# Optimization experiments

Hardware: AMD Instinct MI355X
Metric: run time of the kernel (lower is better)

The kernel has to match this reference:

```python
import jax, jax.numpy as jnp
import numpy as np

B = 32768   # batch
D = 1024    # input_dimension
H = 2048    # hidden width (layer_sizes = [2048, 2048])
LN_EPS = 1e-5


def _layer_norm(h, g, b):
    m = jnp.mean(h, axis=-1, keepdims=True)
    v = jnp.var(h, axis=-1, keepdims=True)
    return (h - m) * jax.lax.rsqrt(v + LN_EPS) * g + b


def setup_inputs() -> dict:
    key = jax.random.key(0)
    ks = jax.random.split(key, 5)
    s1 = 1.0 / np.sqrt(D)
    s2 = 1.0 / np.sqrt(H)
    return {
        "x": jax.random.normal(ks[0], (B, D), dtype=jnp.float32),
        "W1": jax.random.uniform(ks[1], (D, H), jnp.float32, -s1, s1),
        "b1": jax.random.uniform(ks[2], (H,), jnp.float32, -s1, s1),
        "g1": jnp.ones((H,), jnp.float32),
        "be1": jnp.zeros((H,), jnp.float32),
        "W2": jax.random.uniform(ks[3], (H, 9), jnp.float32, -s2, s2),
        "b2": jax.random.uniform(ks[4], (9,), jnp.float32, -s2, s2),
        "g2": jnp.ones((9,), jnp.float32),
        "be2": jnp.zeros((9,), jnp.float32),
    }


def reference(x, W1, b1, g1, be1, W2, b2, g2, be2):
    # MLP: Linear -> ReLU -> LayerNorm, twice (final width 9)
    h = _layer_norm(jax.nn.relu(x @ W1 + b1), g1, be1)      # [B, H]
    r = _layer_norm(jax.nn.relu(h @ W2 + b2), g2, be2)      # [B, 9]
    R = r.reshape(x.shape[0], 3, 3)                          # [B, 3, 3]
    # SVD projection onto SO(3): U @ diag(1,1,det(U Vh)) @ Vh
    U, _, Vh = jnp.linalg.svd(R, full_matrices=False)
    d = jnp.linalg.det(U @ Vh)                               # [B]
    scale = jnp.stack([jnp.ones_like(d), jnp.ones_like(d), d], axis=-1)  # [B,3]
    return (U * scale[:, None, :]) @ Vh                      # scale last col of U
```

## Files before the change

### kernel.cpp

```cpp
#include <hip/hip_runtime.h>

typedef unsigned short u16;
typedef _Float16 f16x8 __attribute__((ext_vector_type(8)));
typedef float f32x4 __attribute__((ext_vector_type(4)));

#define GLD16(gptr, lptr)                                                              \
  __builtin_amdgcn_global_load_lds((const __attribute__((address_space(1))) void*)(gptr), \
                                   (__attribute__((address_space(3))) void*)(lptr), 16, 0, 0)

#define MFMA_F16(a, b, c) __builtin_amdgcn_mfma_f32_16x16x32_f16((a), (b), (c), 0, 0, 0)

__global__ __launch_bounds__(256) void k_split_w1t(const float* __restrict__ w1,
                                                   u16* __restrict__ wh, u16* __restrict__ wl) {
  __shared__ float tile[32][33];
  int bn = blockIdx.x & 63;
  int bk = blockIdx.x >> 6;
  int tn = threadIdx.x & 31, tq = threadIdx.x >> 5;
#pragma unroll
  for (int r = 0; r < 4; ++r) {
    int k = bk * 32 + tq + r * 8;
    tile[tq + r * 8][tn] = w1[(size_t)k * 2048 + bn * 32 + tn];
  }
  __syncthreads();
#pragma unroll
  for (int r = 0; r < 4; ++r) {
    int n = bn * 32 + tq + r * 8;
    float v = tile[tn][tq + r * 8];
    _Float16 hi = (_Float16)v;
    _Float16 lo = (_Float16)(v - (float)hi);
    int qp = (tn >> 3) ^ ((n >> 1) & 3);
    int kp = bk * 32 + qp * 8 + (tn & 7);
    wh[(size_t)n * 1024 + kp] = __builtin_bit_cast(u16, hi);
    wl[(size_t)n * 1024 + kp] = __builtin_bit_cast(u16, lo);
  }
}

__global__ __launch_bounds__(256) void k_w2frag(const float* __restrict__ w2, const float* __restrict__ g1,
                                                u16* __restrict__ fh, u16* __restrict__ fl) {
  int t = blockIdx.x * 256 + threadIdx.x;
  int c = t >> 6, l = t & 63;
  int col = l & 15, lg = l >> 4;
  f16x8 H, L;
#pragma unroll
  for (int j = 0; j < 8; ++j) {
    int k = c * 32 + lg * 8 + j;
    float v = (col < 9) ? g1[k] * w2[k * 9 + col] : 0.f;
    _Float16 hi = (_Float16)v;
    H[j] = hi;
    L[j] = (_Float16)(v - (float)hi);
  }
  *(f16x8*)(fh + (size_t)t * 8) = H;
  *(f16x8*)(fl + (size_t)t * 8) = L;
}

__global__ void k_cgcb(const float* __restrict__ w2, const float* __restrict__ g1,
                       const float* __restrict__ be1, double* __restrict__ cgcb) {
  int l = threadIdx.x;
  double cg[9], cb[9];
#pragma unroll
  for (int j = 0; j < 9; ++j) { cg[j] = 0.0; cb[j] = 0.0; }
  for (int i = 0; i < 32; ++i) {
    int k = i * 64 + l;
    double g = (double)g1[k], b = (double)be1[k];
#pragma unroll
    for (int j = 0; j < 9; ++j) {
      double w = (double)w2[k * 9 + j];
      cg[j] += g * w;
      cb[j] += b * w;
    }
  }
  for (int off = 32; off; off >>= 1) {
#pragma unroll
    for (int j = 0; j < 9; ++j) {
      cg[j] += __shfl_xor(cg[j], off, 64);
      cb[j] += __shfl_xor(cb[j], off, 64);
    }
  }
  if (l == 0) {
    for (int j = 0; j < 16; ++j) {
      cgcb[j] = (j < 9) ? cg[j] : 0.0;
      cgcb[16 + j] = (j < 9) ? cb[j] : 0.0;
    }
  }
}

__global__ __launch_bounds__(512, 2) void k_gemm1(const float* __restrict__ x,
                                                  const u16* __restrict__ wh, const u16* __restrict__ wl,
                                                  const float* __restrict__ b1,
                                                  const u16* __restrict__ fh, const u16* __restrict__ fl,
                                                  float* __restrict__ pdot, float* __restrict__ pstat) {
  __shared__ __align__(16) u16 lds[2][4][8192];
  const int tid = threadIdx.x;
  const int swz = ((blockIdx.x & 7) << 7) | (blockIdx.x >> 3);
  const int m0 = (swz >> 3) << 8;
  const int n0 = (swz & 7) << 8;
  const int lane = tid & 63, w = tid >> 6;
  const int wr = (w >> 2) << 7;
  const int wc = (w & 3) << 6;
  const int lr = lane & 15, lg = lane >> 4;

  int a_off[8], b_off[4];
#pragma unroll
  for (int i = 0; i < 8; ++i) {
    int row = wr + i * 16 + lr;
    a_off[i] = row * 32 + ((lg ^ ((row >> 1) & 3)) << 3);
  }
#pragma unroll
  for (int j = 0; j < 4; ++j) {
    int row = wc + j * 16 + lr;
    b_off[j] = row * 32 + ((lg ^ ((row >> 1) & 3)) << 3);
  }

  const size_t sxa_lo = (size_t)(m0 + (tid >> 2)) * 1024 + (size_t)(((tid & 3) ^ ((tid >> 3) & 3)) << 3);
  const size_t sxa_hi = sxa_lo + (size_t)128 * 1024;
  const size_t boff = (size_t)(n0 + (tid >> 2)) * 1024 + ((tid & 3) << 3);

#define STAGE_B(bf, mt, src, kk)                                          \
  do {                                                                    \
    GLD16((src) + boff + (kk), &lds[bf][mt][tid * 8]);                    \
    GLD16((src) + boff + 131072 + (kk), &lds[bf][mt][4096 + tid * 8]);    \
  } while (0)

#define LOAD_A(REG, kk)                                                   \
  do {                                                                    \
    REG[0] = *(const float4*)(x + sxa_lo + (kk));                         \
    REG[1] = *(const float4*)(x + sxa_lo + (kk) + 4);                     \
    REG[2] = *(const float4*)(x + sxa_hi + (kk));                         \
    REG[3] = *(const float4*)(x + sxa_hi + (kk) + 4);                     \
  } while (0)

#define CVT_STORE(bf, REG)                                                \
  do {                                                                    \
    float ff0[8] = {REG[0].x, REG[0].y, REG[0].z, REG[0].w,               \
                    REG[1].x, REG[1].y, REG[1].z, REG[1].w};              \
    float ff1[8] = {REG[2].x, REG[2].y, REG[2].z, REG[2].w,               \
                    REG[3].x, REG[3].y, REG[3].z, REG[3].w};              \
    f16x8 H0, L0, H1, L1;                                                 \
    _Pragma("unroll")                                                     \
    for (int e = 0; e < 8; ++e) {                                         \
      _Float16 h0 = (_Float16)ff0[e];                                     \
      H0[e] = h0;                                                         \
      L0[e] = (_Float16)(ff0[e] - (float)h0);                             \
      _Float16 h1 = (_Float16)ff1[e];                                     \
      H1[e] = h1;                                                         \
      L1[e] = (_Float16)(ff1[e] - (float)h1);                             \
    }                                                                     \
    *(f16x8*)&lds[bf][0][tid * 8] = H0;                                   \
    *(f16x8*)&lds[bf][1][tid * 8] = L0;                                   \
    *(f16x8*)&lds[bf][0][4096 + tid * 8] = H1;                            \
    *(f16x8*)&lds[bf][1][4096 + tid * 8] = L1;                            \
  } while (0)

  float4 regA[4], regB[4];

  LOAD_A(regA, 0);
  LOAD_A(regB, 32);
  STAGE_B(0, 2, wh, 0);
  STAGE_B(0, 3, wl, 0);
  asm volatile("s_waitcnt vmcnt(8)" ::: "memory");
  CVT_STORE(0, regA);

  f32x4 acc[8][4] = {};

#define RD_B(CUR, j)                                      \
  do {                                                    \
    bhf[j] = *(const f16x8*)(&lds[CUR][2][0] + b_off[j]); \
    blf[j] = *(const f16x8*)(&lds[CUR][3][0] + b_off[j]); \
  } while (0)
#define RD_A(CUR, s, i)                                   \
  do {                                                    \
    ahf[s] = *(const f16x8*)(&lds[CUR][0][0] + a_off[i]); \
    alf[s] = *(const f16x8*)(&lds[CUR][1][0] + a_off[i]); \
  } while (0)
#define MM(s, i, j)                                       \
  do {                                                    \
    acc[i][j] = MFMA_F16(ahf[s], bhf[j], acc[i][j]);      \
    acc[i][j] = MFMA_F16(ahf[s], blf[j], acc[i][j]);      \
    acc[i][j] = MFMA_F16(alf[s], bhf[j], acc[i][j]);      \
  } while (0)
#define PRIO1 __builtin_amdgcn_s_setprio(1)
#define PRIO0 __builtin_amdgcn_s_setprio(0)

#define KBODY(KT, CUR, NXT, RLOAD, RCVT)                                            \
  do {                                                                              \
    const int nk1 = ((KT) + 1 < 32 ? (KT) + 1 : 31) * 32;                           \
    const int nk2 = ((KT) + 2 < 32 ? (KT) + 2 : 31) * 32;                           \
    LOAD_A(RLOAD, nk2);                                        \
    asm volatile("s_waitcnt vmcnt(8)" ::: "memory");        \
    CVT_STORE(NXT, RCVT);                                  \
    asm volatile("s_waitcnt vmcnt(4)" ::: "memory");              \
    __builtin_amdgcn_s_barrier();                         \
    asm volatile("" ::: "memory");                                                  \
    f16x8 bhf[4], blf[4], ahf[4], alf[4];                                           \
    RD_B(CUR, 0); RD_A(CUR, 0, 0);                                                  \
    PRIO1; MM(0, 0, 0); PRIO0;                                                      \
    RD_A(CUR, 1, 1);                                                                \
    PRIO1; MM(1, 1, 0); PRIO0;                                                      \
    RD_B(CUR, 1);                                                                   \
    PRIO1; MM(0, 0, 1); MM(1, 1, 1); PRIO0;                                         \
    RD_A(CUR, 2, 2);                                                                \
    PRIO1; MM(2, 2, 0); MM(2, 2, 1); PRIO0;                                         \
    RD_A(CUR, 3, 3);                                                                \
    PRIO1; MM(3, 3, 0); MM(3, 3, 1); PRIO0;                                         \
    RD_B(CUR, 2);                                                                   \
    STAGE_B(NXT, 2, wh, nk1);                                                       \
    PRIO1; MM(0, 0, 2); MM(1, 1, 2); MM(2, 2, 2); MM(3, 3, 2); PRIO0;               \
    RD_B(CUR, 3);                                                                   \
    STAGE_B(NXT, 3, wl, nk1);                                                       \
    PRIO1; MM(0, 0, 3); MM(1, 1, 3); MM(2, 2, 3); MM(3, 3, 3); PRIO0;               \
    RD_A(CUR, 0, 4);                                                                \
    PRIO1; MM(0, 4, 0); MM(0, 4, 1); MM(0, 4, 2); MM(0, 4, 3); PRIO0;               \
    RD_A(CUR, 1, 5);                                                                \
    PRIO1; MM(1, 5, 0); MM(1, 5, 1); MM(1, 5, 2); MM(1, 5, 3); PRIO0;               \
    RD_A(CUR, 2, 6);                                                                \
    PRIO1; MM(2, 6, 0); MM(2, 6, 1); MM(2, 6, 2); MM(2, 6, 3); PRIO0;               \
    RD_A(CUR, 3, 7);                                                                \
    PRIO1; MM(3, 7, 0); MM(3, 7, 1); MM(3, 7, 2); MM(3, 7, 3); PRIO0;               \
    asm volatile("" ::: "memory");                                                  \
    __builtin_amdgcn_s_barrier();              \
  } while (0)

  for (int kt2 = 0; kt2 < 16; ++kt2) {
    KBODY(2 * kt2,     0, 1, regA, regB);
    KBODY(2 * kt2 + 1, 1, 0, regB, regA);
  }
#undef KBODY
#undef RD_B
#undef RD_A
#undef MM
#undef PRIO1
#undef PRIO0
#undef STAGE_B
#undef LOAD_A
#undef CVT_STORE

  asm volatile("s_waitcnt vmcnt(0)" ::: "memory");
  __syncthreads();
  float* vt = (float*)&lds[0][0][0];

#pragma unroll
  for (int j = 0; j < 4; ++j) {
    const float bias = b1[n0 + wc + j * 16 + lr];
#pragma unroll
    for (int i = 0; i < 8; ++i)
#pragma unroll
      for (int r = 0; r < 4; ++r) acc[i][j][r] = fmaxf(acc[i][j][r] + bias, 0.f);
  }

  f32x4 acc2[2] = {};
  float sstat[2] = {0.f, 0.f}, qstat[2] = {0.f, 0.f};
  const int myrow0 = w * 32;

#pragma unroll
  for (int half = 0; half < 2; ++half) {
    if (((w & 3) >> 1) == half) {
      const int colbase = wc & 127;
#pragma unroll
      for (int j = 0; j < 4; ++j) {
        const int lcol = colbase + j * 16 + lr;
        const int g = lcol >> 2, wsel = lcol & 3;
#pragma unroll
        for (int i = 0; i < 8; ++i)
#pragma unroll
          for (int r = 0; r < 4; ++r) {
            const int row = wr + i * 16 + lg * 4 + r;
            vt[row * 128 + ((g ^ (row & 7)) << 2) + wsel] = acc[i][j][r];
          }
      }
    }
    __syncthreads();
#pragma unroll
    for (int cl = 0; cl < 4; ++cl) {
      const int cglob = (n0 >> 5) + half * 4 + cl;
      const f16x8 bh = *(const f16x8*)(fh + (size_t)(cglob * 64 + lane) * 8);
      const f16x8 bl = *(const f16x8*)(fl + (size_t)(cglob * 64 + lane) * 8);
#pragma unroll
      for (int g2 = 0; g2 < 2; ++g2) {
        const int row = myrow0 + g2 * 16 + lr;
        const int g0 = cl * 8 + lg * 2;
        const float4 f0 = *(const float4*)&vt[row * 128 + ((g0 ^ (row & 7)) << 2)];
        const float4 f1 = *(const float4*)&vt[row * 128 + (((g0 + 1) ^ (row & 7)) << 2)];
        float f[8] = {f0.x, f0.y, f0.z, f0.w, f1.x, f1.y, f1.z, f1.w};
        f16x8 AH, AL;
#pragma unroll
        for (int e = 0; e < 8; ++e) {
          sstat[g2] += f[e];
          qstat[g2] = fmaf(f[e], f[e], qstat[g2]);
          _Float16 hi = (_Float16)f[e];
          AH[e] = hi;
          AL[e] = (_Float16)(f[e] - (float)hi);
        }
        acc2[g2] = MFMA_F16(AH, bh, acc2[g2]);
        acc2[g2] = MFMA_F16(AH, bl, acc2[g2]);
        acc2[g2] = MFMA_F16(AL, bh, acc2[g2]);
      }
    }
    __syncthreads();
  }

#pragma unroll
  for (int g2 = 0; g2 < 2; ++g2) {
    sstat[g2] += __shfl_xor(sstat[g2], 16, 64);
    sstat[g2] += __shfl_xor(sstat[g2], 32, 64);
    qstat[g2] += __shfl_xor(qstat[g2], 16, 64);
    qstat[g2] += __shfl_xor(qstat[g2], 32, 64);
  }
  const int ntile = n0 >> 8;
#pragma unroll
  for (int g2 = 0; g2 < 2; ++g2) {
    if (lg == 0) {
      const int row = m0 + myrow0 + g2 * 16 + lr;
      *(float2*)&pstat[((size_t)row * 8 + ntile) * 2] = make_float2(sstat[g2], qstat[g2]);
    }
    if (lr < 9) {
#pragma unroll
      for (int r = 0; r < 4; ++r) {
        const int row = m0 + myrow0 + g2 * 16 + lg * 4 + r;
        pdot[((size_t)row * 8 + ntile) * 12 + lr] = acc2[g2][r];
      }
    }
  }
}

static __device__ __forceinline__ void jrot(double S[3][3], double V[3][3], int p, int q, int r) {
  double apq = S[p][q];
  if (apq == 0.0) return;
  double tau = (S[q][q] - S[p][p]) / (2.0 * apq);
  double t = (tau >= 0.0 ? 1.0 : -1.0) / (fabs(tau) + sqrt(1.0 + tau * tau));
  double c = 1.0 / sqrt(1.0 + t * t);
  double s = t * c;
  double spp = S[p][p], sqq = S[q][q];
  double srp = S[r][p], srq = S[r][q];
  S[p][p] = spp - t * apq;
  S[q][q] = sqq + t * apq;
  S[p][q] = 0.0; S[q][p] = 0.0;
  S[r][p] = c * srp - s * srq; S[p][r] = S[r][p];
  S[r][q] = s * srp + c * srq; S[q][r] = S[r][q];
#pragma unroll
  for (int i = 0; i < 3; ++i) {
    double vip = V[i][p], viq = V[i][q];
    V[i][p] = c * vip - s * viq;
    V[i][q] = s * vip + c * viq;
  }
}

static __device__ void svd_so3(const double* Rf, float* Of) {
  double A[3][3], S[3][3];
  double V[3][3] = {{1, 0, 0}, {0, 1, 0}, {0, 0, 1}};
#pragma unroll
  for (int i = 0; i < 3; ++i)
#pragma unroll
    for (int j = 0; j < 3; ++j) A[i][j] = Rf[i * 3 + j];
#pragma unroll
  for (int p = 0; p < 3; ++p)
#pragma unroll
    for (int q = 0; q < 3; ++q) {
      double sa = 0.0;
#pragma unroll
      for (int i = 0; i < 3; ++i) sa += A[i][p] * A[i][q];
      S[p][q] = sa;
    }
  for (int it = 0; it < 6; ++it) {
    jrot(S, V, 0, 1, 2);
    jrot(S, V, 0, 2, 1);
    jrot(S, V, 1, 2, 0);
  }
  double l0 = S[0][0], l1 = S[1][1], l2 = S[2][2];
  double c0[3] = {V[0][0], V[1][0], V[2][0]};
  double c1[3] = {V[0][1], V[1][1], V[2][1]};
  double c2[3] = {V[0][2], V[1][2], V[2][2]};
  double tl, tv;
#define SWP(la, lb, ca, cb)                                         \
  if (la < lb) {                                                    \
    tl = la; la = lb; lb = tl;                                      \
    tv = ca[0]; ca[0] = cb[0]; cb[0] = tv;                          \
    tv = ca[1]; ca[1] = cb[1]; cb[1] = tv;                          \
    tv = ca[2]; ca[2] = cb[2]; cb[2] = tv;                          \
  }
  SWP(l0, l1, c0, c1)
  SWP(l0, l2, c0, c2)
  SWP(l1, l2, c1, c2)
#undef SWP
  double v3[3];
  v3[0] = c0[1] * c1[2] - c0[2] * c1[1];
  v3[1] = c0[2] * c1[0] - c0[0] * c1[2];
  v3[2] = c0[0] * c1[1] - c0[1] * c1[0];
  double t1[3], t2[3];
#pragma unroll
  for (int i = 0; i < 3; ++i) {
    t1[i] = A[i][0] * c0[0] + A[i][1] * c0[1] + A[i][2] * c0[2];
    t2[i] = A[i][0] * c1[0] + A[i][1] * c1[1] + A[i][2] * c1[2];
  }
  double n1 = sqrt(t1[0] * t1[0] + t1[1] * t1[1] + t1[2] * t1[2]);
  if (n1 < 1e-20) {
#pragma unroll
    for (int t = 0; t < 9; ++t) Of[t] = (t == 0 || t == 4 || t == 8) ? 1.f : 0.f;
    return;
  }
  double u1[3], u2[3], u3[3];
  double r1 = 1.0 / n1;
#pragma unroll
  for (int i = 0; i < 3; ++i) u1[i] = t1[i] * r1;
  double d12 = u1[0] * t2[0] + u1[1] * t2[1] + u1[2] * t2[2];
#pragma unroll
  for (int i = 0; i < 3; ++i) t2[i] -= d12 * u1[i];
  double n2 = sqrt(t2[0] * t2[0] + t2[1] * t2[1] + t2[2] * t2[2]);
  if (n2 > 1e-14 * n1) {
    double r2 = 1.0 / n2;
#pragma unroll
    for (int i = 0; i < 3; ++i) u2[i] = t2[i] * r2;
  } else {
    double ax = fabs(u1[0]), ay = fabs(u1[1]), az = fabs(u1[2]);
    double e[3] = {0.0, 0.0, 0.0};
    if (ax <= ay && ax <= az) e[0] = 1.0;
    else if (ay <= az) e[1] = 1.0;
    else e[2] = 1.0;
    double d = e[0] * u1[0] + e[1] * u1[1] + e[2] * u1[2];
#pragma unroll
    for (int i = 0; i < 3; ++i) e[i] -= d * u1[i];
    double nn = 1.0 / sqrt(e[0] * e[0] + e[1] * e[1] + e[2] * e[2]);
#pragma unroll
    for (int i = 0; i < 3; ++i) u2[i] = e[i] * nn;
  }
  u3[0] = u1[1] * u2[2] - u1[2] * u2[1];
  u3[1] = u1[2] * u2[0] - u1[0] * u2[2];
  u3[2] = u1[0] * u2[1] - u1[1] * u2[0];
#pragma unroll
  for (int i = 0; i < 3; ++i)
#pragma unroll
    for (int j = 0; j < 3; ++j)
      Of[i * 3 + j] = (float)(u1[i] * c0[j] + u2[i] * c1[j] + u3[i] * v3[j]);
}

__global__ __launch_bounds__(256) void k_comb(const float* __restrict__ pdot,
                                              const float* __restrict__ pstat,
                                              const double* __restrict__ cgcb,
                                              const float* __restrict__ b2,
                                              const float* __restrict__ g2v,
                                              const float* __restrict__ be2,
                                              float* __restrict__ out) {
  const int row = blockIdx.x * 256 + threadIdx.x;
  double dj[9];
#pragma unroll
  for (int j = 0; j < 9; ++j) dj[j] = 0.0;
  double s = 0.0, q = 0.0;
#pragma unroll
  for (int nt = 0; nt < 8; ++nt) {
    const float* p = pdot + ((size_t)row * 8 + nt) * 12;
#pragma unroll
    for (int j = 0; j < 9; ++j) dj[j] += (double)p[j];
    const float* ps = pstat + ((size_t)row * 8 + nt) * 2;
    s += (double)ps[0];
    q += (double)ps[1];
  }
  const double mean = s * (1.0 / 2048.0);
  const double varr = fmax(q * (1.0 / 2048.0) - mean * mean, 0.0);
  const double inv = 1.0 / sqrt(varr + 1e-5);
  double a2[9];
  double s9 = 0.0, q9 = 0.0;
#pragma unroll
  for (int j = 0; j < 9; ++j) {
    double v = inv * (dj[j] - mean * cgcb[j]) + cgcb[16 + j] + (double)b2[j];
    v = fmax(v, 0.0);
    a2[j] = v;
    s9 += v;
    q9 += v * v;
  }
  const double m2 = s9 * (1.0 / 9.0);
  const double v2c = fmax(q9 * (1.0 / 9.0) - m2 * m2, 0.0);
  const double i2 = 1.0 / sqrt(v2c + 1e-5);
  double rn[9];
#pragma unroll
  for (int j = 0; j < 9; ++j) rn[j] = (a2[j] - m2) * i2 * (double)g2v[j] + (double)be2[j];
  float O[9];
  svd_so3(rn, O);
  float* op = out + (size_t)row * 9;
#pragma unroll
  for (int t = 0; t < 9; ++t) op[t] = O[t];
}

extern "C" void kernel_launch(void* const* d_in, const int* in_sizes, int n_in,
                              void* d_out, int out_size, void* d_ws, size_t ws_size,
                              hipStream_t stream) {
  const float* x   = (const float*)d_in[0];
  const float* W1  = (const float*)d_in[1];
  const float* b1  = (const float*)d_in[2];
  const float* g1  = (const float*)d_in[3];
  const float* be1 = (const float*)d_in[4];
  const float* W2  = (const float*)d_in[5];
  const float* b2  = (const float*)d_in[6];
  const float* g2  = (const float*)d_in[7];
  const float* be2 = (const float*)d_in[8];
  float* out = (float*)d_out;
  char* ws = (char*)d_ws;
  u16*    wh   = (u16*)(ws + 0);
  u16*    wl   = (u16*)(ws + 4194304);
  u16*    fh   = (u16*)(ws + 8388608);
  u16*    fl   = (u16*)(ws + 8454144);
  double* cgcb = (double*)(ws + 8519680);
  float*  pdot = (float*)(ws + 8519936);
  float*  pstat= (float*)(ws + 21102848);

  k_split_w1t<<<dim3(2048), dim3(256), 0, stream>>>(W1, wh, wl);
  k_w2frag<<<dim3(16), dim3(256), 0, stream>>>(W2, g1, fh, fl);
  k_cgcb<<<dim3(1), dim3(64), 0, stream>>>(W2, g1, be1, cgcb);
  k_gemm1<<<dim3(1024), dim3(512), 0, stream>>>(x, wh, wl, b1, fh, fl, pdot, pstat);
  k_comb<<<dim3(128), dim3(256), 0, stream>>>(pdot, pstat, cgcb, b2, g2, be2, out);
}
```

Measured before the change: 392.8 us.

## Use 1024-thread blocks in GEMM1 with smaller per-wave tiles and simpler pipeline

The GEMM1 kernel moves from 512 to 1024 threads per block, so each of 16 waves computes a 64x64 sub-tile instead of 128x64. The accumulator count per thread halves. The A and B staging loads are spread across twice as many threads, and the explicit two-stage register ping-pong with fine-grained MFMA/LDS interleaving is replaced by a simpler loop that loads the next step and converts at the end. This lowers register pressure and adds more waves for latency hiding. In exchange, A-fragment reuse per wave drops, and the prefetch depth and interleaving that hid global and LDS latency are reduced, with more vmcnt(0) waits at each barrier.

New measurement: 437.1 us. +11.3%, slower.

```diff
diff --git a/kernel.cpp b/kernel.cpp
--- a/kernel.cpp
+++ b/kernel.cpp
@@ -84,24 +84,24 @@
   }
 }
 
-__global__ __launch_bounds__(512, 2) void k_gemm1(const float* __restrict__ x,
-                                                  const u16* __restrict__ wh, const u16* __restrict__ wl,
-                                                  const float* __restrict__ b1,
-                                                  const u16* __restrict__ fh, const u16* __restrict__ fl,
-                                                  float* __restrict__ pdot, float* __restrict__ pstat) {
+__global__ __launch_bounds__(1024) void k_gemm1(const float* __restrict__ x,
+                                                const u16* __restrict__ wh, const u16* __restrict__ wl,
+                                                const float* __restrict__ b1,
+                                                const u16* __restrict__ fh, const u16* __restrict__ fl,
+                                                float* __restrict__ pdot, float* __restrict__ pstat) {
   __shared__ __align__(16) u16 lds[2][4][8192];
   const int tid = threadIdx.x;
   const int swz = ((blockIdx.x & 7) << 7) | (blockIdx.x >> 3);
   const int m0 = (swz >> 3) << 8;
   const int n0 = (swz & 7) << 8;
   const int lane = tid & 63, w = tid >> 6;
-  const int wr = (w >> 2) << 7;
+  const int wr = (w >> 2) << 6;
   const int wc = (w & 3) << 6;
   const int lr = lane & 15, lg = lane >> 4;
 
-  int a_off[8], b_off[4];
-#pragma unroll
-  for (int i = 0; i < 8; ++i) {
+  int a_off[4], b_off[4];
+#pragma unroll
+  for (int i = 0; i < 4; ++i) {
     int row = wr + i * 16 + lr;
     a_off[i] = row * 32 + ((lg ^ ((row >> 1) & 3)) << 3);
   }
@@ -111,126 +111,96 @@
     b_off[j] = row * 32 + ((lg ^ ((row >> 1) & 3)) << 3);
   }
 
-  const size_t sxa_lo = (size_t)(m0 + (tid >> 2)) * 1024 + (size_t)(((tid & 3) ^ ((tid >> 3) & 3)) << 3);
-  const size_t sxa_hi = sxa_lo + (size_t)128 * 1024;
+  const size_t sxa = (size_t)(m0 + (tid >> 2)) * 1024 + (size_t)(((tid & 3) ^ ((tid >> 3) & 3)) << 3);
   const size_t boff = (size_t)(n0 + (tid >> 2)) * 1024 + ((tid & 3) << 3);
 
-#define STAGE_B(bf, mt, src, kk)                                          \
+#define LOAD_A(kk)                                                        \
   do {                                                                    \
-    GLD16((src) + boff + (kk), &lds[bf][mt][tid * 8]);                    \
-    GLD16((src) + boff + 131072 + (kk), &lds[bf][mt][4096 + tid * 8]);    \
+    regA0 = *(const float4*)(x + sxa + (kk));                             \
+    regA1 = *(const float4*)(x + sxa + (kk) + 4);                         \
   } while (0)
 
-#define LOAD_A(REG, kk)                                                   \
+#define CVT_STORE(bf)                                                     \
   do {                                                                    \
-    REG[0] = *(const float4*)(x + sxa_lo + (kk));                         \
-    REG[1] = *(const float4*)(x + sxa_lo + (kk) + 4);                     \
-    REG[2] = *(const float4*)(x + sxa_hi + (kk));                         \
-    REG[3] = *(const float4*)(x + sxa_hi + (kk) + 4);                     \
-  } while (0)
-
-#define CVT_STORE(bf, REG)                                                \
-  do {                                                                    \
-    float ff0[8] = {REG[0].x, REG[0].y, REG[0].z, REG[0].w,               \
-                    REG[1].x, REG[1].y, REG[1].z, REG[1].w};              \
-    float ff1[8] = {REG[2].x, REG[2].y, REG[2].z, REG[2].w,               \
-                    REG[3].x, REG[3].y, REG[3].z, REG[3].w};              \
-    f16x8 H0, L0, H1, L1;                                                 \
+    float ff[8] = {regA0.x, regA0.y, regA0.z, regA0.w,                    \
+                   regA1.x, regA1.y, regA1.z, regA1.w};                   \
+    f16x8 H, L;                                                           \
     _Pragma("unroll")                                                     \
     for (int e = 0; e < 8; ++e) {                                         \
-      _Float16 h0 = (_Float16)ff0[e];                                     \
-      H0[e] = h0;                                                         \
-      L0[e] = (_Float16)(ff0[e] - (float)h0);                             \
-      _Float16 h1 = (_Float16)ff1[e];                                     \
-      H1[e] = h1;                                                         \
-      L1[e] = (_Float16)(ff1[e] - (float)h1);                             \
+      _Float16 h = (_Float16)ff[e];                                       \
+      H[e] = h;                                                           \
+      L[e] = (_Float16)(ff[e] - (float)h);                                \
     }                                                                     \
-    *(f16x8*)&lds[bf][0][tid * 8] = H0;                                   \
-    *(f16x8*)&lds[bf][1][tid * 8] = L0;                                   \
-    *(f16x8*)&lds[bf][0][4096 + tid * 8] = H1;                            \
-    *(f16x8*)&lds[bf][1][4096 + tid * 8] = L1;                            \
+    *(f16x8*)&lds[bf][0][tid * 8] = H;                                    \
+    *(f16x8*)&lds[bf][1][tid * 8] = L;                                    \
   } while (0)
 
-  float4 regA[4], regB[4];
-
-  LOAD_A(regA, 0);
-  LOAD_A(regB, 32);
-  STAGE_B(0, 2, wh, 0);
-  STAGE_B(0, 3, wl, 0);
-  asm volatile("s_waitcnt vmcnt(8)" ::: "memory");
-  CVT_STORE(0, regA);
-
-  f32x4 acc[8][4] = {};
-
-#define RD_B(CUR, j)                                      \
+  float4 regA0, regA1;
+
+  LOAD_A(0);
+  asm volatile("s_waitcnt vmcnt(0)" ::: "memory");
+  CVT_STORE(0);
+  GLD16(wh + boff, &lds[0][2][tid * 8]);
+  GLD16(wl + boff, &lds[0][3][tid * 8]);
+  asm volatile("s_waitcnt lgkmcnt(0)" ::: "memory");
+
+  f32x4 acc[4][4] = {};
+
+#define RD_B(j)                                           \
   do {                                                    \
-    bhf[j] = *(const f16x8*)(&lds[CUR][2][0] + b_off[j]); \
-    blf[j] = *(const f16x8*)(&lds[CUR][3][0] + b_off[j]); \
+    bhf[j] = *(const f16x8*)(Bh + b_off[j]);              \
+    blf[j] = *(const f16x8*)(Bl + b_off[j]);              \
   } while (0)
-#define RD_A(CUR, s, i)                                   \
+#define RD_A(i)                                           \
   do {                                                    \
-    ahf[s] = *(const f16x8*)(&lds[CUR][0][0] + a_off[i]); \
-    alf[s] = *(const f16x8*)(&lds[CUR][1][0] + a_off[i]); \
+    ahf = *(const f16x8*)(Ah + a_off[i]);                 \
+    alf = *(const f16x8*)(Al + a_off[i]);                 \
   } while (0)
-#define MM(s, i, j)                                       \
+#define MM(i, j)                                          \
   do {                                                    \
-    acc[i][j] = MFMA_F16(ahf[s], bhf[j], acc[i][j]);      \
-    acc[i][j] = MFMA_F16(ahf[s], blf[j], acc[i][j]);      \
-    acc[i][j] = MFMA_F16(alf[s], bhf[j], acc[i][j]);      \
+    acc[i][j] = MFMA_F16(ahf, bhf[j], acc[i][j]);         \
+    acc[i][j] = MFMA_F16(ahf, blf[j], acc[i][j]);         \
+    acc[i][j] = MFMA_F16(alf, bhf[j], acc[i][j]);         \
   } while (0)
 #define PRIO1 __builtin_amdgcn_s_setprio(1)
 #define PRIO0 __builtin_amdgcn_s_setprio(0)
 
-#define KBODY(KT, CUR, NXT, RLOAD, RCVT)                                            \
-  do {                                                                              \
-    const int nk1 = ((KT) + 1 < 32 ? (KT) + 1 : 31) * 32;                           \
-    const int nk2 = ((KT) + 2 < 32 ? (KT) + 2 : 31) * 32;                           \
-    LOAD_A(RLOAD, nk2);                                        \
-    asm volatile("s_waitcnt vmcnt(8)" ::: "memory");        \
-    CVT_STORE(NXT, RCVT);                                  \
-    asm volatile("s_waitcnt vmcnt(4)" ::: "memory");              \
-    __builtin_amdgcn_s_barrier();                         \
-    asm volatile("" ::: "memory");                                                  \
-    f16x8 bhf[4], blf[4], ahf[4], alf[4];                                           \
-    RD_B(CUR, 0); RD_A(CUR, 0, 0);                                                  \
-    PRIO1; MM(0, 0, 0); PRIO0;                                                      \
-    RD_A(CUR, 1, 1);                                                                \
-    PRIO1; MM(1, 1, 0); PRIO0;                                                      \
-    RD_B(CUR, 1);                                                                   \
-    PRIO1; MM(0, 0, 1); MM(1, 1, 1); PRIO0;                                         \
-    RD_A(CUR, 2, 2);                                                                \
-    PRIO1; MM(2, 2, 0); MM(2, 2, 1); PRIO0;                                         \
-    RD_A(CUR, 3, 3);                                                                \
-    PRIO1; MM(3, 3, 0); MM(3, 3, 1); PRIO0;                                         \
-    RD_B(CUR, 2);                                                                   \
-    STAGE_B(NXT, 2, wh, nk1);                                                       \
-    PRIO1; MM(0, 0, 2); MM(1, 1, 2); MM(2, 2, 2); MM(3, 3, 2); PRIO0;               \
-    RD_B(CUR, 3);                                                                   \
-    STAGE_B(NXT, 3, wl, nk1);                                                       \
-    PRIO1; MM(0, 0, 3); MM(1, 1, 3); MM(2, 2, 3); MM(3, 3, 3); PRIO0;               \
-    RD_A(CUR, 0, 4);                                                                \
-    PRIO1; MM(0, 4, 0); MM(0, 4, 1); MM(0, 4, 2); MM(0, 4, 3); PRIO0;               \
-    RD_A(CUR, 1, 5);                                                                \
-    PRIO1; MM(1, 5, 0); MM(1, 5, 1); MM(1, 5, 2); MM(1, 5, 3); PRIO0;               \
-    RD_A(CUR, 2, 6);                                                                \
-    PRIO1; MM(2, 6, 0); MM(2, 6, 1); MM(2, 6, 2); MM(2, 6, 3); PRIO0;               \
-    RD_A(CUR, 3, 7);                                                                \
-    PRIO1; MM(3, 7, 0); MM(3, 7, 1); MM(3, 7, 2); MM(3, 7, 3); PRIO0;               \
-    asm volatile("" ::: "memory");                                                  \
-    __builtin_amdgcn_s_barrier();              \
-  } while (0)
-
-  for (int kt2 = 0; kt2 < 16; ++kt2) {
-    KBODY(2 * kt2,     0, 1, regA, regB);
-    KBODY(2 * kt2 + 1, 1, 0, regB, regA);
-  }
-#undef KBODY
+  for (int kt = 0; kt < 32; ++kt) {
+    const int cur = kt & 1, nxt = cur ^ 1;
+    const int nk1 = ((kt + 1 < 32) ? kt + 1 : 31) * 32;
+    asm volatile("s_waitcnt vmcnt(0)" ::: "memory");
+    __builtin_amdgcn_s_barrier();
+    asm volatile("" ::: "memory");
+    const u16* Ah = &lds[cur][0][0];
+    const u16* Al = &lds[cur][1][0];
+    const u16* Bh = &lds[cur][2][0];
+    const u16* Bl = &lds[cur][3][0];
+    f16x8 bhf[4], blf[4], ahf, alf;
+    LOAD_A(nk1);
+    RD_B(0); RD_B(1);
+    RD_A(0);
+    PRIO1; MM(0, 0); MM(0, 1); PRIO0;
+    RD_B(2); RD_B(3);
+    PRIO1; MM(0, 2); MM(0, 3); PRIO0;
+    RD_A(1);
+    GLD16(wh + boff + nk1, &lds[nxt][2][tid * 8]);
+    PRIO1; MM(1, 0); MM(1, 1); MM(1, 2); MM(1, 3); PRIO0;
+    RD_A(2);
+    GLD16(wl + boff + nk1, &lds[nxt][3][tid * 8]);
+    PRIO1; MM(2, 0); MM(2, 1); MM(2, 2); MM(2, 3); PRIO0;
+    RD_A(3);
+    PRIO1; MM(3, 0); MM(3, 1); MM(3, 2); MM(3, 3); PRIO0;
+    asm volatile("s_waitcnt vmcnt(2)" ::: "memory");
+    CVT_STORE(nxt);
+    asm volatile("s_waitcnt lgkmcnt(0)" ::: "memory");
+    asm volatile("" ::: "memory");
+    __builtin_amdgcn_s_barrier();
+  }
 #undef RD_B
 #undef RD_A
 #undef MM
 #undef PRIO1
 #undef PRIO0
-#undef STAGE_B
 #undef LOAD_A
 #undef CVT_STORE
 
@@ -242,14 +212,14 @@
   for (int j = 0; j < 4; ++j) {
     const float bias = b1[n0 + wc + j * 16 + lr];
 #pragma unroll
-    for (int i = 0; i < 8; ++i)
+    for (int i = 0; i < 4; ++i)
 #pragma unroll
       for (int r = 0; r < 4; ++r) acc[i][j][r] = fmaxf(acc[i][j][r] + bias, 0.f);
   }
 
-  f32x4 acc2[2] = {};
-  float sstat[2] = {0.f, 0.f}, qstat[2] = {0.f, 0.f};
-  const int myrow0 = w * 32;
+  f32x4 acc2 = {0.f, 0.f, 0.f, 0.f};
+  float sstat = 0.f, qstat = 0.f;
+  const int myrow0 = w * 16;
 
 #pragma unroll
   for (int half = 0; half < 2; ++half) {
@@ -260,7 +230,7 @@
         const int lcol = colbase + j * 16 + lr;
         const int g = lcol >> 2, wsel = lcol & 3;
 #pragma unroll
-        for (int i = 0; i < 8; ++i)
+        for (int i = 0; i < 4; ++i)
 #pragma unroll
           for (int r = 0; r < 4; ++r) {
             const int row = wr + i * 16 + lg * 4 + r;
@@ -274,50 +244,41 @@
       const int cglob = (n0 >> 5) + half * 4 + cl;
       const f16x8 bh = *(const f16x8*)(fh + (size_t)(cglob * 64 + lane) * 8);
       const f16x8 bl = *(const f16x8*)(fl + (size_t)(cglob * 64 + lane) * 8);
-#pragma unroll
-      for (int g2 = 0; g2 < 2; ++g2) {
-        const int row = myrow0 + g2 * 16 + lr;
-        const int g0 = cl * 8 + lg * 2;
-        const float4 f0 = *(const float4*)&vt[row * 128 + ((g0 ^ (row & 7)) << 2)];
-        const float4 f1 = *(const float4*)&vt[row * 128 + (((g0 + 1) ^ (row & 7)) << 2)];
-        float f[8] = {f0.x, f0.y, f0.z, f0.w, f1.x, f1.y, f1.z, f1.w};
-        f16x8 AH, AL;
-#pragma unroll
-        for (int e = 0; e < 8; ++e) {
-          sstat[g2] += f[e];
-          qstat[g2] = fmaf(f[e], f[e], qstat[g2]);
-          _Float16 hi = (_Float16)f[e];
-          AH[e] = hi;
-          AL[e] = (_Float16)(f[e] - (float)hi);
-        }
-        acc2[g2] = MFMA_F16(AH, bh, acc2[g2]);
-        acc2[g2] = MFMA_F16(AH, bl, acc2[g2]);
-        acc2[g2] = MFMA_F16(AL, bh, acc2[g2]);
+      const int row = myrow0 + lr;
+      const int g0 = cl * 8 + lg * 2;
+      const float4 f0 = *(const float4*)&vt[row * 128 + ((g0 ^ (row & 7)) << 2)];
+      const float4 f1 = *(const float4*)&vt[row * 128 + (((g0 + 1) ^ (row & 7)) << 2)];
+      float f[8] = {f0.x, f0.y, f0.z, f0.w, f1.x, f1.y, f1.z, f1.w};
+      f16x8 AH, AL;
+#pragma unroll
+      for (int e = 0; e < 8; ++e) {
+        sstat += f[e];
+        qstat = fmaf(f[e], f[e], qstat);
+        _Float16 hi = (_Float16)f[e];
+        AH[e] = hi;
+        AL[e] = (_Float16)(f[e] - (float)hi);
       }
+      acc2 = MFMA_F16(AH, bh, acc2);
+      acc2 = MFMA_F16(AH, bl, acc2);
+      acc2 = MFMA_F16(AL, bh, acc2);
     }
     __syncthreads();
   }
 
-#pragma unroll
-  for (int g2 = 0; g2 < 2; ++g2) {
-    sstat[g2] += __shfl_xor(sstat[g2], 16, 64);
-    sstat[g2] += __shfl_xor(sstat[g2], 32, 64);
-    qstat[g2] += __shfl_xor(qstat[g2], 16, 64);
-    qstat[g2] += __shfl_xor(qstat[g2], 32, 64);
-  }
+  sstat += __shfl_xor(sstat, 16, 64);
+  sstat += __shfl_xor(sstat, 32, 64);
+  qstat += __shfl_xor(qstat, 16, 64);
+  qstat += __shfl_xor(qstat, 32, 64);
   const int ntile = n0 >> 8;
-#pragma unroll
-  for (int g2 = 0; g2 < 2; ++g2) {
-    if (lg == 0) {
-      const int row = m0 + myrow0 + g2 * 16 + lr;
-      *(float2*)&pstat[((size_t)row * 8 + ntile) * 2] = make_float2(sstat[g2], qstat[g2]);
-    }
-    if (lr < 9) {
-#pragma unroll
-      for (int r = 0; r < 4; ++r) {
-        const int row = m0 + myrow0 + g2 * 16 + lg * 4 + r;
-        pdot[((size_t)row * 8 + ntile) * 12 + lr] = acc2[g2][r];
-      }
+  if (lg == 0) {
+    const int row = m0 + myrow0 + lr;
+    *(float2*)&pstat[((size_t)row * 8 + ntile) * 2] = make_float2(sstat, qstat);
+  }
+  if (lr < 9) {
+#pragma unroll
+    for (int r = 0; r < 4; ++r) {
+      const int row = m0 + myrow0 + lg * 4 + r;
+      pdot[((size_t)row * 8 + ntile) * 12 + lr] = acc2[r];
     }
   }
 }
@@ -504,6 +465,6 @@
   k_split_w1t<<<dim3(2048), dim3(256), 0, stream>>>(W1, wh, wl);
   k_w2frag<<<dim3(16), dim3(256), 0, stream>>>(W2, g1, fh, fl);
   k_cgcb<<<dim3(1), dim3(64), 0, stream>>>(W2, g1, be1, cgcb);
-  k_gemm1<<<dim3(1024), dim3(512), 0, stream>>>(x, wh, wl, b1, fh, fl, pdot, pstat);
+  k_gemm1<<<dim3(1024), dim3(1024), 0, stream>>>(x, wh, wl, b1, fh, fl, pdot, pstat);
   k_comb<<<dim3(128), dim3(256), 0, stream>>>(pdot, pstat, cgcb, b2, g2, be2, out);
 }
```
